# Performance work log

Hardware: AMD Instinct MI355X
Metric: run time of the kernel (lower is better)

Reference implementation:

```python
import jax, jax.numpy as jnp
import numpy as np

EPS = 1e-12

def _normalize(v):
    # matches F.normalize(..., eps): v / max(||v||, eps)
    return v / jnp.maximum(jnp.linalg.norm(v), EPS)

def sn_weight(W, u):
    """One power iteration (num_svs=1, num_itrs=1, eval mode: u not updated).
    W: [out, in] (1x1 conv flattened). u: [1, out].
    u, v are no-grad in torch; sv = v @ W.T @ u'.T carries grad w.r.t. W."""
    v = jax.lax.stop_gradient(_normalize(jax.lax.stop_gradient(u) @ W))          # [1, in]
    u2 = jax.lax.stop_gradient(_normalize(v @ W.T))                              # [1, out]
    sv = (v @ W.T @ u2.T)[0, 0]
    return W / sv

def maxpool2x2(x):
    B, C, H, W = x.shape
    return x.reshape(B, C, H // 2, 2, W // 2, 2).max(axis=(3, 5))

def conv1x1(W, x):
    # W: [out_c, in_c], x: [B, in_c, H, W]
    return jnp.einsum('oc,bchw->bohw', W, x)

def setup_inputs() -> dict:
    key = jax.random.key(0)
    ks = jax.random.split(key, 9)
    ch = 128
    B, H, W = 16, 64, 64
    x = jax.random.normal(ks[0], (B, ch, H, W), dtype=jnp.float32)
    # 1x1 conv weights flattened to [out, in], kaiming-ish scale
    def w(k, o, i):
        return jax.random.normal(k, (o, i), dtype=jnp.float32) * (1.0 / np.sqrt(i))
    w_theta = w(ks[1], ch // 8, ch)
    w_phi   = w(ks[2], ch // 8, ch)
    w_g     = w(ks[3], ch // 2, ch)
    w_o     = w(ks[4], ch, ch // 2)
    u_theta = jax.random.normal(ks[5], (1, ch // 8), dtype=jnp.float32)
    u_phi   = jax.random.normal(ks[6], (1, ch // 8), dtype=jnp.float32)
    u_g     = jax.random.normal(ks[7], (1, ch // 2), dtype=jnp.float32)
    u_o     = jax.random.normal(ks[8], (1, ch), dtype=jnp.float32)
    gamma = jnp.float32(0.7)  # param (init 0.0 in torch; nonzero for a meaningful test)
    return dict(x=x, w_theta=w_theta, w_phi=w_phi, w_g=w_g, w_o=w_o,
                u_theta=u_theta, u_phi=u_phi, u_g=u_g, u_o=u_o, gamma=gamma)

def reference(x, w_theta, w_phi, w_g, w_o, u_theta, u_phi, u_g, u_o, gamma):
    B, C, H, W = x.shape
    Wt = sn_weight(w_theta, u_theta)
    Wp = sn_weight(w_phi, u_phi)
    Wg = sn_weight(w_g, u_g)
    Wo = sn_weight(w_o, u_o)
    theta = conv1x1(Wt, x).reshape(B, C // 8, H * W)               # [B, C/8, HW]
    phi = maxpool2x2(conv1x1(Wp, x)).reshape(B, C // 8, H * W // 4)  # [B, C/8, HW/4]
    g = maxpool2x2(conv1x1(Wg, x)).reshape(B, C // 2, H * W // 4)    # [B, C/2, HW/4]
    beta = jax.nn.softmax(jnp.einsum('bcs,bct->bst', theta, phi), axis=-1)  # [B, HW, HW/4]
    o = jnp.einsum('bct,bst->bcs', g, beta).reshape(B, C // 2, H, W)
    return gamma * conv1x1(Wo, o) + x
```

## Files before the change

### kernel.cpp

```cpp
#include <hip/hip_runtime.h>
#include <hip/hip_bf16.h>


#define U_WN  0
#define U_WO  12288
#define U_TH  20480
#define U_PHI 1069056
#define U_G   1331200
#define U_OT  2379776

typedef __attribute__((ext_vector_type(8))) short bf16x8;
typedef __attribute__((ext_vector_type(4))) short s16x4;
typedef __attribute__((ext_vector_type(4))) float f32x4;
typedef __attribute__((ext_vector_type(16))) float f32x16;

__device__ inline unsigned short f2b(float f) {
    union { float f; unsigned u; } v; v.f = f;
    unsigned r = v.u + 0x7FFFu + ((v.u >> 16) & 1u);
    return (unsigned short)(r >> 16);
}
__device__ inline float b2f(unsigned short u) {
    union { unsigned u; float f; } v; v.u = ((unsigned)u) << 16; return v.f;
}

__device__ inline unsigned cvtpk_bf16(float lo, float hi) {
    unsigned r;
    asm("s_nop 0\n\tv_cvt_pk_bf16_f32 %0, %1, %2" : "=v"(r) : "v"(lo), "v"(hi));
    return r;
}
__device__ inline void pl32swap(unsigned &a, unsigned &b) {
    asm("s_nop 1\n\tv_permlane32_swap_b32 %0, %1\n\ts_nop 1" : "+v"(a), "+v"(b));
}

__global__ __launch_bounds__(256) void sn4(
        const float* __restrict__ w0, const float* __restrict__ w1,
        const float* __restrict__ w2, const float* __restrict__ w3,
        const float* __restrict__ u0, const float* __restrict__ u1,
        const float* __restrict__ u2, const float* __restrict__ u3,
        unsigned short* __restrict__ wsu) {
    int wi = blockIdx.x;
    const float* W; const float* u; unsigned short* dst; int on, in_;
    if      (wi == 0) { W = w0; u = u0; dst = wsu;          on = 16;  in_ = 128; }
    else if (wi == 1) { W = w1; u = u1; dst = wsu + 2048;   on = 16;  in_ = 128; }
    else if (wi == 2) { W = w2; u = u2; dst = wsu + 4096;   on = 64;  in_ = 128; }
    else              { W = w3; u = u3; dst = wsu + 12288;  on = 128; in_ = 64;  }
    __shared__ float Wl[8320];
    __shared__ float ul[128];
    __shared__ float v[128];
    __shared__ float red[256];
    __shared__ float s_inv;
    int tid = threadIdx.x;
    int n = on * in_;
    int stride = in_ + 1;
    int shift = (in_ == 128) ? 7 : 6;
    int mask = in_ - 1;
    for (int i = tid; i < n; i += 256) {
        int o = i >> shift, j = i & mask;
        Wl[o * stride + j] = W[i];
    }
    if (tid < on) ul[tid] = u[tid];
    __syncthreads();
    float vi = 0.f;
    if (tid < in_) {
        for (int o = 0; o < on; ++o) vi += ul[o] * Wl[o * stride + tid];
    }
    red[tid] = (tid < in_) ? vi * vi : 0.f;
    __syncthreads();
    for (int st = 128; st > 0; st >>= 1) {
        if (tid < st) red[tid] += red[tid + st];
        __syncthreads();
    }
    float inv_nv = 1.0f / fmaxf(sqrtf(red[0]), 1e-12f);
    __syncthreads();
    if (tid < in_) v[tid] = vi * inv_nv;
    __syncthreads();
    float ui = 0.f;
    if (tid < on) {
        for (int i = 0; i < in_; ++i) ui += v[i] * Wl[tid * stride + i];
    }
    red[tid] = (tid < on) ? ui * ui : 0.f;
    __syncthreads();
    for (int st = 128; st > 0; st >>= 1) {
        if (tid < st) red[tid] += red[tid + st];
        __syncthreads();
    }
    if (tid == 0) {
        float nsq = red[0];
        float sv = nsq / fmaxf(sqrtf(nsq), 1e-12f);
        s_inv = 1.0f / sv;
    }
    __syncthreads();
    float inv = s_inv;
    for (int e = tid; e < n; e += 256) {
        int o = e >> shift, j = e & mask;
        dst[e] = f2b(Wl[o * stride + j] * inv);
    }
}

__global__ __launch_bounds__(256, 2) void convpool_mfma(
        const float* __restrict__ x, const unsigned short* __restrict__ wn,
        unsigned short* __restrict__ thetaT, unsigned short* __restrict__ phiT,
        unsigned short* __restrict__ gT) {
    __shared__ unsigned short xT[128 * 136];
    __shared__ unsigned short wnl[96 * 136];
    int tid = threadIdx.x;
    int bb = blockIdx.x >> 5, tile = blockIdx.x & 31;
    int px0 = tile << 7;
    for (int i = tid; i < 1536; i += 256) {
        int r = i >> 4, c8 = (i & 15) * 8;
        *(bf16x8*)&wnl[r * 136 + c8] = *(const bf16x8*)&wn[r * 128 + c8];
    }
    const float4* x4 = (const float4*)x;
    {
        int p4 = tid & 31, cg = (tid >> 5) * 4;
        for (int k = 0; k < 4; ++k) {
            int cb = k * 32 + cg;
            float4 v0 = x4[(bb * 128 + cb + 0) * 1024 + tile * 32 + p4];
            float4 v1 = x4[(bb * 128 + cb + 1) * 1024 + tile * 32 + p4];
            float4 v2 = x4[(bb * 128 + cb + 2) * 1024 + tile * 32 + p4];
            float4 v3 = x4[(bb * 128 + cb + 3) * 1024 + tile * 32 + p4];
            float a0[4] = {v0.x, v0.y, v0.z, v0.w};
            float a1[4] = {v1.x, v1.y, v1.z, v1.w};
            float a2[4] = {v2.x, v2.y, v2.z, v2.w};
            float a3[4] = {v3.x, v3.y, v3.z, v3.w};
#pragma unroll
            for (int j = 0; j < 4; ++j) {
                union { unsigned w[2]; s16x4 v; } pk;
                pk.w[0] = cvtpk_bf16(a0[j], a1[j]);
                pk.w[1] = cvtpk_bf16(a2[j], a3[j]);
                *(s16x4*)&xT[(p4 * 4 + j) * 136 + cb] = pk.v;
            }
        }
    }
    __syncthreads();
    int lane = tid & 63, wv = tid >> 6;
    int q = lane >> 4, l = lane & 15;
    int pxw = wv * 32;
    f32x4 acc[2][6];
    const f32x4 z4 = {0.f, 0.f, 0.f, 0.f};
#pragma unroll
    for (int mt = 0; mt < 2; ++mt)
#pragma unroll
        for (int nt = 0; nt < 6; ++nt) acc[mt][nt] = z4;
#pragma unroll
    for (int kk = 0; kk < 4; ++kk) {
        bf16x8 a0 = *(const bf16x8*)&xT[(pxw + l) * 136 + kk * 32 + q * 8];
        bf16x8 a1 = *(const bf16x8*)&xT[(pxw + 16 + l) * 136 + kk * 32 + q * 8];
#pragma unroll
        for (int nt = 0; nt < 6; ++nt) {
            bf16x8 bw = *(const bf16x8*)&wnl[(nt * 16 + l) * 136 + kk * 32 + q * 8];
            acc[0][nt] = __builtin_amdgcn_mfma_f32_16x16x32_bf16(a0, bw, acc[0][nt], 0, 0, 0);
            acc[1][nt] = __builtin_amdgcn_mfma_f32_16x16x32_bf16(a1, bw, acc[1][nt], 0, 0, 0);
        }
    }
#pragma unroll
    for (int mt = 0; mt < 2; ++mt)
#pragma unroll
        for (int r = 0; r < 4; ++r) {
            int s = px0 + pxw + mt * 16 + q * 4 + r;
            thetaT[(bb * 4096 + s) * 16 + l] = f2b(acc[mt][0][r]);
        }
    __syncthreads();
    unsigned short* poolbuf = wnl;
#pragma unroll
    for (int mt = 0; mt < 2; ++mt)
#pragma unroll
        for (int nt = 1; nt < 6; ++nt) {
            int ch = nt * 16 + l - 16;
#pragma unroll
            for (int r = 0; r < 4; ++r) {
                poolbuf[ch * 132 + pxw + mt * 16 + q * 4 + r] = f2b(acc[mt][nt][r]);
            }
        }
    __syncthreads();
    for (int i = tid; i < 2560; i += 256) {
        int tcol = i & 31, ch = i >> 5;
        int base = ch * 132 + tcol * 2;
        float m0 = fmaxf(b2f(poolbuf[base]), b2f(poolbuf[base + 1]));
        float m1 = fmaxf(b2f(poolbuf[base + 64]), b2f(poolbuf[base + 65]));
        float m = fmaxf(m0, m1);
        int t = tile * 32 + tcol;
        if (ch < 16) phiT[(bb * 1024 + t) * 16 + ch] = f2b(m);
        else         gT[(bb * 64 + ch - 16) * 1024 + t] = f2b(m);
    }
}

__global__ __launch_bounds__(512, 4) void attn_mfma(
        const unsigned short* __restrict__ thetaT,
        const unsigned short* __restrict__ phiT,
        const unsigned short* __restrict__ gT,
        unsigned short* __restrict__ oT) {
    __shared__ float ldsO[4][2048];
    __shared__ float ldsD[4][32];
    int tid = threadIdx.x;
    int kblk = blockIdx.x;
    int vblk = (kblk & 7) * 64 + (kblk >> 3);
    int bb = vblk >> 5, st = vblk & 31;
    int s0 = st << 7;
    int lane = tid & 63, wv = tid >> 6;
    int sg = wv & 3, sp = wv >> 2;
    int sl = lane & 31, hi = lane >> 5;
    int srow = bb * 4096 + s0 + sg * 32 + sl;
    const unsigned short* phiB = phiT + bb * 16384;
    const unsigned short* gB   = gT + bb * 65536;
    int tbase = sp << 9;

    bf16x8 bth = *(const bf16x8*)&thetaT[srow * 16 + hi * 8];

    f32x16 z16;
#pragma unroll
    for (int i = 0; i < 16; ++i) z16[i] = 0.f;
    f32x16 acc0 = z16, acc1 = z16;
    float lp4[4] = {0.f, 0.f, 0.f, 0.f};

    bf16x8 ph0 = *(const bf16x8*)&phiB[(tbase + sl) * 16 + hi * 8];
    bf16x8 ph1 = *(const bf16x8*)&phiB[(tbase + 32 + sl) * 16 + hi * 8];

    for (int tc = 0; tc < 8; ++tc) {
        int t0 = tbase + (tc << 6);
        bf16x8 gf0[4], gf1[4];
#pragma unroll
        for (int kt = 0; kt < 4; ++kt) {
            gf0[kt] = *(const bf16x8*)&gB[(sl) * 1024 + t0 + kt * 16 + hi * 8];
            gf1[kt] = *(const bf16x8*)&gB[(32 + sl) * 1024 + t0 + kt * 16 + hi * 8];
        }
        f32x16 sa0 = __builtin_amdgcn_mfma_f32_32x32x16_bf16(ph0, bth, z16, 0, 0, 0);
        f32x16 sa1 = __builtin_amdgcn_mfma_f32_32x32x16_bf16(ph1, bth, z16, 0, 0, 0);
        int t0n = tbase + (((tc + 1) & 7) << 6);
        ph0 = *(const bf16x8*)&phiB[(t0n + sl) * 16 + hi * 8];
        ph1 = *(const bf16x8*)&phiB[(t0n + 32 + sl) * 16 + hi * 8];
        unsigned u0[8], u1[8];
#pragma unroll
        for (int i = 0; i < 8; ++i) {
            float e0 = __expf(sa0[2 * i]);
            float e1 = __expf(sa0[2 * i + 1]);
            float e2 = __expf(sa1[2 * i]);
            float e3 = __expf(sa1[2 * i + 1]);
            lp4[0] += e0; lp4[1] += e1; lp4[2] += e2; lp4[3] += e3;
            u0[i] = cvtpk_bf16(e0, e1);
            u1[i] = cvtpk_bf16(e2, e3);
        }
        pl32swap(u0[0], u0[2]); pl32swap(u0[1], u0[3]);
        pl32swap(u0[4], u0[6]); pl32swap(u0[5], u0[7]);
        pl32swap(u1[0], u1[2]); pl32swap(u1[1], u1[3]);
        pl32swap(u1[4], u1[6]); pl32swap(u1[5], u1[7]);
        {
            union { unsigned w[4]; bf16x8 v; } pf = {{u0[0], u0[1], u0[2], u0[3]}};
            acc0 = __builtin_amdgcn_mfma_f32_32x32x16_bf16(gf0[0], pf.v, acc0, 0, 0, 0);
            acc1 = __builtin_amdgcn_mfma_f32_32x32x16_bf16(gf1[0], pf.v, acc1, 0, 0, 0);
        }
        {
            union { unsigned w[4]; bf16x8 v; } pf = {{u0[4], u0[5], u0[6], u0[7]}};
            acc0 = __builtin_amdgcn_mfma_f32_32x32x16_bf16(gf0[1], pf.v, acc0, 0, 0, 0);
            acc1 = __builtin_amdgcn_mfma_f32_32x32x16_bf16(gf1[1], pf.v, acc1, 0, 0, 0);
        }
        {
            union { unsigned w[4]; bf16x8 v; } pf = {{u1[0], u1[1], u1[2], u1[3]}};
            acc0 = __builtin_amdgcn_mfma_f32_32x32x16_bf16(gf0[2], pf.v, acc0, 0, 0, 0);
            acc1 = __builtin_amdgcn_mfma_f32_32x32x16_bf16(gf1[2], pf.v, acc1, 0, 0, 0);
        }
        {
            union { unsigned w[4]; bf16x8 v; } pf = {{u1[4], u1[5], u1[6], u1[7]}};
            acc0 = __builtin_amdgcn_mfma_f32_32x32x16_bf16(gf0[3], pf.v, acc0, 0, 0, 0);
            acc1 = __builtin_amdgcn_mfma_f32_32x32x16_bf16(gf1[3], pf.v, acc1, 0, 0, 0);
        }
    }
    float tot = (lp4[0] + lp4[1]) + (lp4[2] + lp4[3]);
    tot += __shfl_xor(tot, 32);

    if (sp == 1) {
#pragma unroll
        for (int i = 0; i < 16; ++i) {
            int c = (i & 3) + 8 * (i >> 2) + 4 * hi;
            ldsO[sg][c * 32 + sl] = acc0[i];
            ldsO[sg][(32 + c) * 32 + sl] = acc1[i];
        }
        if (hi == 0) ldsD[sg][sl] = tot;
    }
    __syncthreads();
    if (sp == 1) return;
    tot += ldsD[sg][sl];
    float inv = 1.0f / tot;
#pragma unroll
    for (int i = 0; i < 16; ++i) {
        int c = (i & 3) + 8 * (i >> 2) + 4 * hi;
        acc0[i] += ldsO[sg][c * 32 + sl];
        acc1[i] += ldsO[sg][(32 + c) * 32 + sl];
    }
    unsigned o0[8], o1[8];
#pragma unroll
    for (int i = 0; i < 8; ++i) {
        o0[i] = cvtpk_bf16(acc0[2 * i] * inv, acc0[2 * i + 1] * inv);
        o1[i] = cvtpk_bf16(acc1[2 * i] * inv, acc1[2 * i + 1] * inv);
    }
    pl32swap(o0[0], o0[2]); pl32swap(o0[1], o0[3]);
    pl32swap(o0[4], o0[6]); pl32swap(o0[5], o0[7]);
    pl32swap(o1[0], o1[2]); pl32swap(o1[1], o1[3]);
    pl32swap(o1[4], o1[6]); pl32swap(o1[5], o1[7]);
    unsigned short* orow = oT + srow * 64;
    {
        union { unsigned w[4]; bf16x8 v; } ow = {{o0[0], o0[1], o0[2], o0[3]}};
        *(bf16x8*)&orow[hi * 8] = ow.v;
    }
    {
        union { unsigned w[4]; bf16x8 v; } ow = {{o0[4], o0[5], o0[6], o0[7]}};
        *(bf16x8*)&orow[16 + hi * 8] = ow.v;
    }
    {
        union { unsigned w[4]; bf16x8 v; } ow = {{o1[0], o1[1], o1[2], o1[3]}};
        *(bf16x8*)&orow[32 + hi * 8] = ow.v;
    }
    {
        union { unsigned w[4]; bf16x8 v; } ow = {{o1[4], o1[5], o1[6], o1[7]}};
        *(bf16x8*)&orow[48 + hi * 8] = ow.v;
    }
}

__global__ __launch_bounds__(256, 2) void outconv_mfma(
        const unsigned short* __restrict__ oT, const unsigned short* __restrict__ wo,
        const float* __restrict__ x, const float* __restrict__ gam,
        float* __restrict__ out) {
    __shared__ unsigned short wol[128 * 72];
    int tid = threadIdx.x;
    int bb = blockIdx.x >> 4, tile = blockIdx.x & 15;
    int lane = tid & 63, wv = tid >> 6;
    int q = lane >> 4, l = lane & 15;
    int pxw = tile * 256 + wv * 64;
    for (int i = tid; i < 1024; i += 256) {
        int r = i >> 3, c8 = (i & 7) * 8;
        *(bf16x8*)&wol[r * 72 + c8] = *(const bf16x8*)&wo[r * 64 + c8];
    }
    bf16x8 af[4][2];
#pragma unroll
    for (int mt = 0; mt < 4; ++mt)
#pragma unroll
        for (int kk = 0; kk < 2; ++kk)
            af[mt][kk] = *(const bf16x8*)&oT[(bb * 4096 + pxw + mt * 16 + l) * 64 + kk * 32 + q * 8];
    __syncthreads();
    f32x4 acc[4][8];
    const f32x4 z4 = {0.f, 0.f, 0.f, 0.f};
#pragma unroll
    for (int mt = 0; mt < 4; ++mt)
#pragma unroll
        for (int nt = 0; nt < 8; ++nt) acc[mt][nt] = z4;
#pragma unroll
    for (int kk = 0; kk < 2; ++kk) {
#pragma unroll
        for (int nt = 0; nt < 8; ++nt) {
            bf16x8 bw = *(const bf16x8*)&wol[(nt * 16 + l) * 72 + kk * 32 + q * 8];
#pragma unroll
            for (int mt = 0; mt < 4; ++mt)
                acc[mt][nt] = __builtin_amdgcn_mfma_f32_16x16x32_bf16(af[mt][kk], bw, acc[mt][nt], 0, 0, 0);
        }
    }
    float gm = gam[0];
    const float4* x4 = (const float4*)x;
    float4* out4 = (float4*)out;
#pragma unroll
    for (int mt = 0; mt < 4; ++mt)
#pragma unroll
        for (int nt = 0; nt < 8; ++nt) {
            int oc = nt * 16 + l;
            int px = pxw + mt * 16 + q * 4;
            int gi = (bb * 128 + oc) * 1024 + (px >> 2);
            float4 xv = x4[gi];
            float4 r;
            r.x = gm * acc[mt][nt][0] + xv.x;
            r.y = gm * acc[mt][nt][1] + xv.y;
            r.z = gm * acc[mt][nt][2] + xv.z;
            r.w = gm * acc[mt][nt][3] + xv.w;
            out4[gi] = r;
        }
}

extern "C" void kernel_launch(void* const* d_in, const int* in_sizes, int n_in,
                              void* d_out, int out_size, void* d_ws, size_t ws_size,
                              hipStream_t stream) {
    const float* x  = (const float*)d_in[0];
    const float* wt = (const float*)d_in[1];
    const float* wp = (const float*)d_in[2];
    const float* wg = (const float*)d_in[3];
    const float* wo = (const float*)d_in[4];
    const float* ut = (const float*)d_in[5];
    const float* up = (const float*)d_in[6];
    const float* ug = (const float*)d_in[7];
    const float* uo = (const float*)d_in[8];
    const float* gm = (const float*)d_in[9];
    unsigned short* wsu = (unsigned short*)d_ws;
    float* out = (float*)d_out;

    sn4<<<4, 256, 0, stream>>>(wt, wp, wg, wo, ut, up, ug, uo, wsu);
    convpool_mfma<<<512, 256, 0, stream>>>(x, wsu + U_WN,
                                           wsu + U_TH, wsu + U_PHI, wsu + U_G);
    attn_mfma<<<512, 512, 0, stream>>>(wsu + U_TH, wsu + U_PHI, wsu + U_G, wsu + U_OT);
    outconv_mfma<<<256, 256, 0, stream>>>(wsu + U_OT, wsu + U_WO, x, gm, out);
}
```

Measured before the change: 163.6 us.

## Raise wave counts in conv kernels and interleave exp with MFMA in attention

The convpool kernel now runs 512 threads per block, with each wave handling 16 pixels instead of 32. The outconv kernel launches four times as many blocks, each covering 64 pixels, which cuts per-thread accumulators and register pressure so more waves can be resident. In the attention loop the two score MFMAs are split so exp on the first half overlaps the second MFMA and part of the g loads. A sched_barrier and s_setprio are added around the PV MFMAs to steer scheduling. The cost is less per-wave reuse of loaded operands and more blocks or redundant weight loads into LDS.

```diff
diff --git a/kernel.cpp b/kernel.cpp
--- a/kernel.cpp
+++ b/kernel.cpp
@@ -97,7 +97,7 @@
     }
 }
 
-__global__ __launch_bounds__(256, 2) void convpool_mfma(
+__global__ __launch_bounds__(512, 4) void convpool_mfma(
         const float* __restrict__ x, const unsigned short* __restrict__ wn,
         unsigned short* __restrict__ thetaT, unsigned short* __restrict__ phiT,
         unsigned short* __restrict__ gT) {
@@ -106,15 +106,15 @@
     int tid = threadIdx.x;
     int bb = blockIdx.x >> 5, tile = blockIdx.x & 31;
     int px0 = tile << 7;
-    for (int i = tid; i < 1536; i += 256) {
+    for (int i = tid; i < 1536; i += 512) {
         int r = i >> 4, c8 = (i & 15) * 8;
         *(bf16x8*)&wnl[r * 136 + c8] = *(const bf16x8*)&wn[r * 128 + c8];
     }
     const float4* x4 = (const float4*)x;
     {
         int p4 = tid & 31, cg = (tid >> 5) * 4;
-        for (int k = 0; k < 4; ++k) {
-            int cb = k * 32 + cg;
+        for (int k = 0; k < 2; ++k) {
+            int cb = k * 64 + cg;
             float4 v0 = x4[(bb * 128 + cb + 0) * 1024 + tile * 32 + p4];
             float4 v1 = x4[(bb * 128 + cb + 1) * 1024 + tile * 32 + p4];
             float4 v2 = x4[(bb * 128 + cb + 2) * 1024 + tile * 32 + p4];
@@ -135,45 +135,37 @@
     __syncthreads();
     int lane = tid & 63, wv = tid >> 6;
     int q = lane >> 4, l = lane & 15;
-    int pxw = wv * 32;
-    f32x4 acc[2][6];
+    int pxw = wv * 16;
+    f32x4 acc[6];
     const f32x4 z4 = {0.f, 0.f, 0.f, 0.f};
 #pragma unroll
-    for (int mt = 0; mt < 2; ++mt)
-#pragma unroll
-        for (int nt = 0; nt < 6; ++nt) acc[mt][nt] = z4;
+    for (int nt = 0; nt < 6; ++nt) acc[nt] = z4;
 #pragma unroll
     for (int kk = 0; kk < 4; ++kk) {
         bf16x8 a0 = *(const bf16x8*)&xT[(pxw + l) * 136 + kk * 32 + q * 8];
-        bf16x8 a1 = *(const bf16x8*)&xT[(pxw + 16 + l) * 136 + kk * 32 + q * 8];
 #pragma unroll
         for (int nt = 0; nt < 6; ++nt) {
             bf16x8 bw = *(const bf16x8*)&wnl[(nt * 16 + l) * 136 + kk * 32 + q * 8];
-            acc[0][nt] = __builtin_amdgcn_mfma_f32_16x16x32_bf16(a0, bw, acc[0][nt], 0, 0, 0);
-            acc[1][nt] = __builtin_amdgcn_mfma_f32_16x16x32_bf16(a1, bw, acc[1][nt], 0, 0, 0);
-        }
-    }
-#pragma unroll
-    for (int mt = 0; mt < 2; ++mt)
+            acc[nt] = __builtin_amdgcn_mfma_f32_16x16x32_bf16(a0, bw, acc[nt], 0, 0, 0);
+        }
+    }
+#pragma unroll
+    for (int r = 0; r < 4; ++r) {
+        int s = px0 + pxw + q * 4 + r;
+        thetaT[(bb * 4096 + s) * 16 + l] = f2b(acc[0][r]);
+    }
+    __syncthreads();
+    unsigned short* poolbuf = wnl;
+#pragma unroll
+    for (int nt = 1; nt < 6; ++nt) {
+        int ch = nt * 16 + l - 16;
 #pragma unroll
         for (int r = 0; r < 4; ++r) {
-            int s = px0 + pxw + mt * 16 + q * 4 + r;
-            thetaT[(bb * 4096 + s) * 16 + l] = f2b(acc[mt][0][r]);
-        }
-    __syncthreads();
-    unsigned short* poolbuf = wnl;
-#pragma unroll
-    for (int mt = 0; mt < 2; ++mt)
-#pragma unroll
-        for (int nt = 1; nt < 6; ++nt) {
-            int ch = nt * 16 + l - 16;
-#pragma unroll
-            for (int r = 0; r < 4; ++r) {
-                poolbuf[ch * 132 + pxw + mt * 16 + q * 4 + r] = f2b(acc[mt][nt][r]);
-            }
-        }
-    __syncthreads();
-    for (int i = tid; i < 2560; i += 256) {
+            poolbuf[ch * 132 + pxw + q * 4 + r] = f2b(acc[nt][r]);
+        }
+    }
+    __syncthreads();
+    for (int i = tid; i < 2560; i += 512) {
         int tcol = i & 31, ch = i >> 5;
         int base = ch * 132 + tcol * 2;
         float m0 = fmaxf(b2f(poolbuf[base]), b2f(poolbuf[base + 1]));
@@ -220,30 +212,41 @@
         int t0 = tbase + (tc << 6);
         bf16x8 gf0[4], gf1[4];
 #pragma unroll
-        for (int kt = 0; kt < 4; ++kt) {
+        for (int kt = 0; kt < 2; ++kt) {
             gf0[kt] = *(const bf16x8*)&gB[(sl) * 1024 + t0 + kt * 16 + hi * 8];
             gf1[kt] = *(const bf16x8*)&gB[(32 + sl) * 1024 + t0 + kt * 16 + hi * 8];
         }
-        f32x16 sa0 = __builtin_amdgcn_mfma_f32_32x32x16_bf16(ph0, bth, z16, 0, 0, 0);
-        f32x16 sa1 = __builtin_amdgcn_mfma_f32_32x32x16_bf16(ph1, bth, z16, 0, 0, 0);
+        f32x16 sa = __builtin_amdgcn_mfma_f32_32x32x16_bf16(ph0, bth, z16, 0, 0, 0);
+        unsigned u0[8], u1[8];
+#pragma unroll
+        for (int i = 0; i < 8; ++i) {
+            float e0 = __expf(sa[2 * i]);
+            float e1 = __expf(sa[2 * i + 1]);
+            lp4[0] += e0; lp4[1] += e1;
+            u0[i] = cvtpk_bf16(e0, e1);
+        }
+        __builtin_amdgcn_sched_barrier(0);
+        f32x16 sb = __builtin_amdgcn_mfma_f32_32x32x16_bf16(ph1, bth, z16, 0, 0, 0);
+        pl32swap(u0[0], u0[2]); pl32swap(u0[1], u0[3]);
+        pl32swap(u0[4], u0[6]); pl32swap(u0[5], u0[7]);
+#pragma unroll
+        for (int kt = 2; kt < 4; ++kt) {
+            gf0[kt] = *(const bf16x8*)&gB[(sl) * 1024 + t0 + kt * 16 + hi * 8];
+            gf1[kt] = *(const bf16x8*)&gB[(32 + sl) * 1024 + t0 + kt * 16 + hi * 8];
+        }
         int t0n = tbase + (((tc + 1) & 7) << 6);
         ph0 = *(const bf16x8*)&phiB[(t0n + sl) * 16 + hi * 8];
         ph1 = *(const bf16x8*)&phiB[(t0n + 32 + sl) * 16 + hi * 8];
-        unsigned u0[8], u1[8];
 #pragma unroll
         for (int i = 0; i < 8; ++i) {
-            float e0 = __expf(sa0[2 * i]);
-            float e1 = __expf(sa0[2 * i + 1]);
-            float e2 = __expf(sa1[2 * i]);
-            float e3 = __expf(sa1[2 * i + 1]);
-            lp4[0] += e0; lp4[1] += e1; lp4[2] += e2; lp4[3] += e3;
-            u0[i] = cvtpk_bf16(e0, e1);
+            float e2 = __expf(sb[2 * i]);
+            float e3 = __expf(sb[2 * i + 1]);
+            lp4[2] += e2; lp4[3] += e3;
             u1[i] = cvtpk_bf16(e2, e3);
         }
-        pl32swap(u0[0], u0[2]); pl32swap(u0[1], u0[3]);
-        pl32swap(u0[4], u0[6]); pl32swap(u0[5], u0[7]);
         pl32swap(u1[0], u1[2]); pl32swap(u1[1], u1[3]);
         pl32swap(u1[4], u1[6]); pl32swap(u1[5], u1[7]);
+        __builtin_amdgcn_s_setprio(1);
         {
             union { unsigned w[4]; bf16x8 v; } pf = {{u0[0], u0[1], u0[2], u0[3]}};
             acc0 = __builtin_amdgcn_mfma_f32_32x32x16_bf16(gf0[0], pf.v, acc0, 0, 0, 0);
@@ -264,6 +267,7 @@
             acc0 = __builtin_amdgcn_mfma_f32_32x32x16_bf16(gf0[3], pf.v, acc0, 0, 0, 0);
             acc1 = __builtin_amdgcn_mfma_f32_32x32x16_bf16(gf1[3], pf.v, acc1, 0, 0, 0);
         }
+        __builtin_amdgcn_s_setprio(0);
     }
     float tot = (lp4[0] + lp4[1]) + (lp4[2] + lp4[3]);
     tot += __shfl_xor(tot, 32);
@@ -316,61 +320,53 @@
     }
 }
 
-__global__ __launch_bounds__(256, 2) void outconv_mfma(
+__global__ __launch_bounds__(256, 4) void outconv_mfma(
         const unsigned short* __restrict__ oT, const unsigned short* __restrict__ wo,
         const float* __restrict__ x, const float* __restrict__ gam,
         float* __restrict__ out) {
     __shared__ unsigned short wol[128 * 72];
     int tid = threadIdx.x;
-    int bb = blockIdx.x >> 4, tile = blockIdx.x & 15;
+    int bb = blockIdx.x >> 6, tile = blockIdx.x & 63;
     int lane = tid & 63, wv = tid >> 6;
     int q = lane >> 4, l = lane & 15;
-    int pxw = tile * 256 + wv * 64;
+    int pxw = tile * 64 + wv * 16;
     for (int i = tid; i < 1024; i += 256) {
         int r = i >> 3, c8 = (i & 7) * 8;
         *(bf16x8*)&wol[r * 72 + c8] = *(const bf16x8*)&wo[r * 64 + c8];
     }
-    bf16x8 af[4][2];
-#pragma unroll
-    for (int mt = 0; mt < 4; ++mt)
-#pragma unroll
-        for (int kk = 0; kk < 2; ++kk)
-            af[mt][kk] = *(const bf16x8*)&oT[(bb * 4096 + pxw + mt * 16 + l) * 64 + kk * 32 + q * 8];
-    __syncthreads();
-    f32x4 acc[4][8];
+    bf16x8 af[2];
+#pragma unroll
+    for (int kk = 0; kk < 2; ++kk)
+        af[kk] = *(const bf16x8*)&oT[(bb * 4096 + pxw + l) * 64 + kk * 32 + q * 8];
+    __syncthreads();
+    f32x4 acc[8];
     const f32x4 z4 = {0.f, 0.f, 0.f, 0.f};
 #pragma unroll
-    for (int mt = 0; mt < 4; ++mt)
-#pragma unroll
-        for (int nt = 0; nt < 8; ++nt) acc[mt][nt] = z4;
+    for (int nt = 0; nt < 8; ++nt) acc[nt] = z4;
 #pragma unroll
     for (int kk = 0; kk < 2; ++kk) {
 #pragma unroll
         for (int nt = 0; nt < 8; ++nt) {
             bf16x8 bw = *(const bf16x8*)&wol[(nt * 16 + l) * 72 + kk * 32 + q * 8];
-#pragma unroll
-            for (int mt = 0; mt < 4; ++mt)
-                acc[mt][nt] = __builtin_amdgcn_mfma_f32_16x16x32_bf16(af[mt][kk], bw, acc[mt][nt], 0, 0, 0);
+            acc[nt] = __builtin_amdgcn_mfma_f32_16x16x32_bf16(af[kk], bw, acc[nt], 0, 0, 0);
         }
     }
     float gm = gam[0];
     const float4* x4 = (const float4*)x;
     float4* out4 = (float4*)out;
 #pragma unroll
-    for (int mt = 0; mt < 4; ++mt)
-#pragma unroll
-        for (int nt = 0; nt < 8; ++nt) {
-            int oc = nt * 16 + l;
-            int px = pxw + mt * 16 + q * 4;
-            int gi = (bb * 128 + oc) * 1024 + (px >> 2);
-            float4 xv = x4[gi];
-            float4 r;
-            r.x = gm * acc[mt][nt][0] + xv.x;
-            r.y = gm * acc[mt][nt][1] + xv.y;
-            r.z = gm * acc[mt][nt][2] + xv.z;
-            r.w = gm * acc[mt][nt][3] + xv.w;
-            out4[gi] = r;
-        }
+    for (int nt = 0; nt < 8; ++nt) {
+        int oc = nt * 16 + l;
+        int px = pxw + q * 4;
+        int gi = (bb * 128 + oc) * 1024 + (px >> 2);
+        float4 xv = x4[gi];
+        float4 r;
+        r.x = gm * acc[nt][0] + xv.x;
+        r.y = gm * acc[nt][1] + xv.y;
+        r.z = gm * acc[nt][2] + xv.z;
+        r.w = gm * acc[nt][3] + xv.w;
+        out4[gi] = r;
+    }
 }
 
 extern "C" void kernel_launch(void* const* d_in, const int* in_sizes, int n_in,
@@ -390,8 +386,8 @@
     float* out = (float*)d_out;
 
     sn4<<<4, 256, 0, stream>>>(wt, wp, wg, wo, ut, up, ug, uo, wsu);
-    convpool_mfma<<<512, 256, 0, stream>>>(x, wsu + U_WN,
+    convpool_mfma<<<512, 512, 0, stream>>>(x, wsu + U_WN,
                                            wsu + U_TH, wsu + U_PHI, wsu + U_G);
     attn_mfma<<<512, 512, 0, stream>>>(wsu + U_TH, wsu + U_PHI, wsu + U_G, wsu + U_OT);
-    outconv_mfma<<<256, 256, 0, stream>>>(wsu + U_OT, wsu + U_WO, x, gm, out);
-}
+    outconv_mfma<<<1024, 256, 0, stream>>>(wsu + U_OT, wsu + U_WO, x, gm, out);
+}
```

New measurement: 154.3 us. 1.06x faster.
